# Kernel optimization log

Measured on AMD Instinct MI355X. Metric: run time of the kernel, lower is better.

Reference implementation:

```python
import jax, jax.numpy as jnp
import numpy as np
from jax import lax

C_IN, C_OUT, H, W = 64, 128, 512, 512


def setup_inputs() -> dict:
    key = jax.random.key(0)
    k1, k2, k3, k4 = jax.random.split(key, 4)
    x = jax.random.normal(k1, (C_IN, H, W), dtype=jnp.float32)
    # Conv2d params (eqx default: kernel 3x3, bias used). Small init scale for stability.
    conv_w = jax.random.normal(k2, (C_OUT, C_IN, 3, 3), dtype=jnp.float32) * 0.05
    conv_b = jax.random.normal(k3, (C_OUT,), dtype=jnp.float32) * 0.05
    fft_mask = jax.random.normal(k4, (C_OUT, H, W), dtype=jnp.float32)
    return {"x": x, "conv_w": conv_w, "conv_b": conv_b, "fft_mask": fft_mask}


def reference(x, conv_w, conv_b, fft_mask):
    # 3x3 same-padding conv on a single (C,H,W) sample -> (C_OUT,H,W)
    y = lax.conv_general_dilated(
        x[None],  # (1,C_IN,H,W)
        conv_w,
        window_strides=(1, 1),
        padding=((1, 1), (1, 1)),
        dimension_numbers=("NCHW", "OIHW", "NCHW"),
    )[0] + conv_b[:, None, None]
    # Per-channel spectral filter: FFT over (H,W), elementwise complex-mask
    # multiply, inverse FFT, take real part. Vectorized over channels.
    Y = jnp.fft.fftn(y, axes=(1, 2)) * fft_mask
    return jnp.fft.ifftn(Y, axes=(1, 2)).real
```

## Files before the change

### kernel.cpp

```cpp
#include <hip/hip_runtime.h>

#define CIN   64
#define COUT  128
#define HH    512
#define WW    512
#define HW    (HH*WW)

typedef __attribute__((ext_vector_type(8))) short  short8;
typedef __attribute__((ext_vector_type(4))) float  floatx4;


__device__ __forceinline__ unsigned short f2bf(float f) {
    unsigned u = __float_as_uint(f);
    u += 0x7fffu + ((u >> 16) & 1u);
    return (unsigned short)(u >> 16);
}

__device__ __forceinline__ void wave_sync() {
    __builtin_amdgcn_wave_barrier();
    asm volatile("s_waitcnt lgkmcnt(0)" ::: "memory");
    __builtin_amdgcn_sched_barrier(0);
}
template<bool BLK> __device__ __forceinline__ void xsync() {
    if (BLK) __syncthreads(); else wave_sync();
}


__global__ __launch_bounds__(256) void k_wprep(
        const float* __restrict__ cw,
        unsigned short* __restrict__ wt)
{
    int i = blockIdx.x * 256 + threadIdx.x;
    int tap = i >> 13;
    int co  = (i >> 6) & 127;
    int ci  = i & 63;
    wt[i] = f2bf(cw[(co * 64 + ci) * 9 + tap]);
}


__global__ __launch_bounds__(256) void k_xprep(
        const float* __restrict__ x,
        unsigned short* __restrict__ xt)
{
    __shared__ unsigned short tile[64][72];
    int t  = threadIdx.x;
    int h  = blockIdx.x >> 3;
    int w0 = (blockIdx.x & 7) << 6;
    int wl = t & 63;
#pragma unroll
    for (int it = 0; it < 16; ++it) {
        int ci = (t >> 6) + 4 * it;
        tile[wl][ci] = f2bf(x[ci * HW + h * 512 + w0 + wl]);
    }
    __syncthreads();
#pragma unroll
    for (int it = 0; it < 2; ++it) {
        int task = t + 256 * it;
        int w = task >> 3, seg = task & 7;
        *(short8*)&xt[((size_t)(h * 512 + w0 + w)) * 64 + seg * 8] =
            *(const short8*)&tile[w][seg * 8];
    }
}


__global__ __launch_bounds__(256) void k_maskT2(
        const float* __restrict__ mask,
        float* __restrict__ mt)
{
    __shared__ float t1[64][65];
    __shared__ float t2[64][65];
    int b  = blockIdx.x;
    int ch = b >> 6;
    int k0 = ((b >> 3) & 7) << 6;
    int c0 = (b & 7) << 6;
    int t  = threadIdx.x;
    int j  = t & 63, i0 = t >> 6;
    const float* mch = mask + (size_t)ch * HW;
#pragma unroll
    for (int it = 0; it < 16; ++it) {
        int i  = i0 + 4 * it;
        int mi = (512 - (k0 + i)) & 511;
        int mj = (512 - (c0 + j)) & 511;
        t1[i][j] = mch[(size_t)(k0 + i) * 512 + (c0 + j)];
        t2[i][j] = mch[(size_t)mi * 512 + mj];
    }
    __syncthreads();
    float* och = mt + (size_t)ch * HW;
#pragma unroll
    for (int it = 0; it < 16; ++it) {
        int jj = i0 + 4 * it;
        och[(size_t)(c0 + jj) * 512 + k0 + j] = t1[j][jj] + t2[j][jj];
    }
}


__global__ __launch_bounds__(512) void k_conv(
        const unsigned short* __restrict__ xt,
        const unsigned short* __restrict__ wt,
        const float* __restrict__ bias,
        float* __restrict__ y)
{
    __shared__ __align__(16) unsigned short As[3][130][68];

    int b  = blockIdx.x;
    int h  = b >> 2;
    int w0 = (b & 3) << 7;
    int t  = threadIdx.x;
    int lane = t & 63, wv = t >> 6;
    int wm = wv >> 2, wn = wv & 3;
    int l15 = lane & 15, quad = lane >> 4;

    for (int idx = t; idx < 3 * 130 * 8; idx += 512) {
        int dy  = idx / 1040;
        int rem = idx - dy * 1040;
        int p   = rem >> 3, seg = rem & 7;
        int hp  = h + dy - 1;
        int wq  = w0 - 1 + p;
        short8 v = {0, 0, 0, 0, 0, 0, 0, 0};
        if ((unsigned)hp < 512u && (unsigned)wq < 512u)
            v = *(const short8*)&xt[((size_t)(hp * 512 + wq)) * 64 + seg * 8];
        *(short8*)&As[dy][p][seg * 8] = v;
    }
    __syncthreads();

    floatx4 acc[4][2];
#pragma unroll
    for (int mt = 0; mt < 4; ++mt)
#pragma unroll
        for (int nt = 0; nt < 2; ++nt) {
            floatx4 z = {0.f, 0.f, 0.f, 0.f};
            acc[mt][nt] = z;
        }

#pragma unroll
    for (int tap = 0; tap < 9; ++tap) {
        int dy = tap / 3, dx = tap - dy * 3;
        short8 bfr[2][2];
#pragma unroll
        for (int nt = 0; nt < 2; ++nt)
#pragma unroll
            for (int kc = 0; kc < 2; ++kc) {
                int co = wn * 32 + nt * 16 + l15;
                bfr[nt][kc] = *(const short8*)
                    &wt[(tap * 128 + co) * 64 + kc * 32 + quad * 8];
            }
#pragma unroll
        for (int kc = 0; kc < 2; ++kc) {
            int c0 = kc * 32 + quad * 8;
            short8 afr[4];
#pragma unroll
            for (int mt = 0; mt < 4; ++mt) {
                int row = wm * 64 + mt * 16 + l15 + dx;
                afr[mt] = *(const short8*)&As[dy][row][c0];
            }
#pragma unroll
            for (int mt = 0; mt < 4; ++mt)
#pragma unroll
                for (int nt = 0; nt < 2; ++nt)
                    acc[mt][nt] = __builtin_amdgcn_mfma_f32_16x16x32_bf16(
                        afr[mt], bfr[nt][kc], acc[mt][nt], 0, 0, 0);
        }
    }

#pragma unroll
    for (int nt = 0; nt < 2; ++nt) {
        int co = wn * 32 + nt * 16 + l15;
        float bv = bias[co];
#pragma unroll
        for (int mt = 0; mt < 4; ++mt) {
            floatx4 o = acc[mt][nt];
            o[0] += bv; o[1] += bv; o[2] += bv; o[3] += bv;
            int m = wm * 64 + mt * 16 + quad * 4;
            *(floatx4*)&y[co * HW + h * 512 + w0 + m] = o;
        }
    }
}


#define FS 576

__device__ __forceinline__ int slotf(int c, int a) {
    return c * FS + ((a + (a >> 3)) ^ c);
}
__device__ __forceinline__ int dr6(int v) {
    return (v >> 3) + 8 * (v & 7);
}

__device__ __forceinline__ float2 cadd(float2 a, float2 b){ return make_float2(a.x+b.x, a.y+b.y); }
__device__ __forceinline__ float2 csub(float2 a, float2 b){ return make_float2(a.x-b.x, a.y-b.y); }

template<int DIR> __device__ __forceinline__ float2 twmul(float2 a, float2 t){
    return (DIR > 0) ? make_float2(a.x*t.x - a.y*t.y, a.x*t.y + a.y*t.x)
                     : make_float2(a.x*t.x + a.y*t.y, a.y*t.x - a.x*t.y);
}
template<int DIR> __device__ __forceinline__ float2 mulJ(float2 a){
    return (DIR > 0) ? make_float2(a.y, -a.x) : make_float2(-a.y, a.x);
}

#define RSQRT2 0.70710678118654752f

template<int DIR> __device__ __forceinline__ void dft8(float2* x){
    float2 a0 = cadd(x[0], x[4]), b0 = csub(x[0], x[4]);
    float2 a1 = cadd(x[1], x[5]), b1 = csub(x[1], x[5]);
    float2 a2 = cadd(x[2], x[6]), b2 = csub(x[2], x[6]);
    float2 a3 = cadd(x[3], x[7]), b3 = csub(x[3], x[7]);
    b1 = (DIR > 0) ? make_float2((b1.x + b1.y)*RSQRT2, (b1.y - b1.x)*RSQRT2)
                   : make_float2((b1.x - b1.y)*RSQRT2, (b1.y + b1.x)*RSQRT2);
    b2 = mulJ<DIR>(b2);
    b3 = (DIR > 0) ? make_float2((b3.y - b3.x)*RSQRT2, -(b3.x + b3.y)*RSQRT2)
                   : make_float2(-(b3.x + b3.y)*RSQRT2, (b3.x - b3.y)*RSQRT2);
    float2 c0 = cadd(a0, a2), d0 = csub(a0, a2);
    float2 c1 = cadd(a1, a3), d1 = mulJ<DIR>(csub(a1, a3));
    x[0] = cadd(c0, c1); x[4] = csub(c0, c1);
    x[2] = cadd(d0, d1); x[6] = csub(d0, d1);
    float2 e0 = cadd(b0, b2), f0 = csub(b0, b2);
    float2 e1 = cadd(b1, b3), f1 = mulJ<DIR>(csub(b1, b3));
    x[1] = cadd(e0, e1); x[5] = csub(e0, e1);
    x[3] = cadd(f0, f1); x[7] = csub(f0, f1);
}

template<bool BLK>
__device__ __forceinline__ void fft512_fwd(float2 X[2][8], float2* buf,
                                           const float2* tw, int w, int c) {
#pragma unroll
    for (int b = 0; b < 2; ++b) {
        dft8<1>(X[b]);
        int g = w + 32*b;
#pragma unroll
        for (int k = 1; k < 8; ++k) X[b][k] = twmul<1>(X[b][k], tw[g*k]);
    }
#pragma unroll
    for (int b = 0; b < 2; ++b) {
        int g = w + 32*b;
#pragma unroll
        for (int k = 0; k < 8; ++k) buf[slotf(c, k*64 + g)] = X[b][k];
    }
    xsync<BLK>();
#pragma unroll
    for (int b = 0; b < 2; ++b) {
        int u = w + 32*b; int bs = (u >> 3)*64 + (u & 7);
#pragma unroll
        for (int g2 = 0; g2 < 8; ++g2) X[b][g2] = buf[slotf(c, bs + 8*g2)];
    }
#pragma unroll
    for (int b = 0; b < 2; ++b) {
        dft8<1>(X[b]);
        int g1 = (w + 32*b) & 7;
#pragma unroll
        for (int k = 1; k < 8; ++k) X[b][k] = twmul<1>(X[b][k], tw[8*g1*k]);
    }
    xsync<BLK>();
#pragma unroll
    for (int b = 0; b < 2; ++b) {
        int u = w + 32*b; int bs = (u >> 3)*64 + (u & 7);
#pragma unroll
        for (int k = 0; k < 8; ++k) buf[slotf(c, bs + 8*k)] = X[b][k];
    }
    xsync<BLK>();
#pragma unroll
    for (int b = 0; b < 2; ++b) {
        int v = w + 32*b;
#pragma unroll
        for (int g1 = 0; g1 < 8; ++g1) X[b][g1] = buf[slotf(c, 8*v + g1)];
    }
#pragma unroll
    for (int b = 0; b < 2; ++b) dft8<1>(X[b]);
}

template<bool BLK>
__device__ __forceinline__ void fft512_inv(float2 X[2][8], float2* buf,
                                           const float2* tw, int w, int c) {
#pragma unroll
    for (int b = 0; b < 2; ++b) dft8<-1>(X[b]);
    xsync<BLK>();
#pragma unroll
    for (int b = 0; b < 2; ++b) {
        int v = w + 32*b;
#pragma unroll
        for (int g1 = 0; g1 < 8; ++g1) buf[slotf(c, 8*v + g1)] = X[b][g1];
    }
    xsync<BLK>();
#pragma unroll
    for (int b = 0; b < 2; ++b) {
        int u = w + 32*b; int bs = (u >> 3)*64 + (u & 7);
#pragma unroll
        for (int k = 0; k < 8; ++k) X[b][k] = buf[slotf(c, bs + 8*k)];
    }
#pragma unroll
    for (int b = 0; b < 2; ++b) {
        int g1 = (w + 32*b) & 7;
#pragma unroll
        for (int k = 1; k < 8; ++k) X[b][k] = twmul<-1>(X[b][k], tw[8*g1*k]);
        dft8<-1>(X[b]);
    }
    xsync<BLK>();
#pragma unroll
    for (int b = 0; b < 2; ++b) {
        int u = w + 32*b; int bs = (u >> 3)*64 + (u & 7);
#pragma unroll
        for (int g2 = 0; g2 < 8; ++g2) buf[slotf(c, bs + 8*g2)] = X[b][g2];
    }
    xsync<BLK>();
#pragma unroll
    for (int b = 0; b < 2; ++b) {
        int g = w + 32*b;
#pragma unroll
        for (int k = 0; k < 8; ++k) X[b][k] = buf[slotf(c, k*64 + g)];
    }
#pragma unroll
    for (int b = 0; b < 2; ++b) {
        int g = w + 32*b;
#pragma unroll
        for (int k = 1; k < 8; ++k) X[b][k] = twmul<-1>(X[b][k], tw[g*k]);
        dft8<-1>(X[b]);
    }
}

__device__ __forceinline__ void build_tw(float2* tw, int t) {
    const float a0 = -6.283185307179586f / 512.0f;
    float s, c;
    __sincosf(a0 * (float)t, &s, &c);         tw[t]       = make_float2(c, s);
    __sincosf(a0 * (float)(t + 256), &s, &c); tw[t + 256] = make_float2(c, s);
}


__global__ __launch_bounds__(256, 4) void k_rows_fwd_pair(
        const float* __restrict__ y,
        float2* __restrict__ Z)
{
    __shared__ float2 buf[8 * FS];
    __shared__ float2 tw[512];
    int t = threadIdx.x;
    build_tw(tw, t);
    int c = t >> 5, w = t & 31;
    int p = blockIdx.x >> 6, r0 = (blockIdx.x & 63) << 3;
    const float* yA = y + (size_t)(2*p) * HW + (size_t)(r0 + c) * 512;
    const float* yB = yA + HW;

    float2 X[2][8];
#pragma unroll
    for (int b = 0; b < 2; ++b)
#pragma unroll
        for (int r = 0; r < 8; ++r) {
            int off = w + 32*b + 64*r;
            X[b][r] = make_float2(yA[off], yB[off]);
        }
    __syncthreads();
    fft512_fwd<false>(X, buf, tw, w, c);

    wave_sync();
#pragma unroll
    for (int b = 0; b < 2; ++b) {
        int kb = dr6(w + 32*b);
#pragma unroll
        for (int m = 0; m < 8; ++m) buf[slotf(c, kb + 64*m)] = X[b][m];
    }
    __syncthreads();
    size_t zb = (size_t)p * HW + r0;
    for (int it = 0; it < 16; ++it) {
        int n = t + 256*it;
        int col = n >> 3, rr = n & 7;
        Z[zb + (size_t)col*512 + rr] = buf[slotf(rr, col)];
    }
}

__device__ __forceinline__ int col_of(int g, int j) {
    if (g == 0) return (j < 4) ? j : (j == 4 ? 256 : 504 + j);
    return (j < 4) ? 4*g + j : 512 - 4*g - 7 + j;
}
__device__ __forceinline__ int jmir(int g, int j) {
    return (g == 0) ? ((8 - j) & 7) : (7 - j);
}

__global__ __launch_bounds__(256, 4) void k_cols_pair(
        float2* __restrict__ Z,
        const float* __restrict__ mt)
{
    __shared__ float2 buf[8 * FS];
    __shared__ float2 tw[512];
    int t = threadIdx.x;
    build_tw(tw, t);
    int c = t >> 5, w = t & 31;
    int p = blockIdx.x >> 6, g = blockIdx.x & 63;
    int colc = col_of(g, c);
    int cm   = jmir(g, c);
    size_t zcol = (size_t)p * HW + (size_t)colc * 512;
    const float* mAp = mt + (size_t)(2*p) * HW + (size_t)colc * 512;
    const float* mBp = mAp + HW;

    float2 X[2][8];
#pragma unroll
    for (int b = 0; b < 2; ++b)
#pragma unroll
        for (int r = 0; r < 8; ++r)
            X[b][r] = Z[zcol + w + 32*b + 64*r];
    float Sa[2][8], Sb[2][8];
#pragma unroll
    for (int b = 0; b < 2; ++b) {
        int kb = dr6(w + 32*b);
#pragma unroll
        for (int m = 0; m < 8; ++m) {
            int k1 = kb + 64*m;
            Sa[b][m] = mAp[k1];
            Sb[b][m] = mBp[k1];
        }
    }
    __syncthreads();
    fft512_fwd<false>(X, buf, tw, w, c);

    wave_sync();
#pragma unroll
    for (int b = 0; b < 2; ++b) {
        int kb = dr6(w + 32*b);
#pragma unroll
        for (int m = 0; m < 8; ++m) buf[slotf(c, kb + 64*m)] = X[b][m];
    }
    __syncthreads();

    const float s4 = 0.25f / 262144.0f;
#pragma unroll
    for (int b = 0; b < 2; ++b) {
        int kb = dr6(w + 32*b);
#pragma unroll
        for (int m = 0; m < 8; ++m) {
            int k1  = kb + 64*m;
            int mk1 = (512 - k1) & 511;
            float2 P = X[b][m];
            float2 Q = buf[slotf(cm, mk1)];
            float alpha = (Sa[b][m] + Sb[b][m]) * s4;
            float beta  = (Sa[b][m] - Sb[b][m]) * s4;
            X[b][m] = make_float2(alpha * P.x + beta * Q.x,
                                  alpha * P.y - beta * Q.y);
        }
    }
    __syncthreads();
    fft512_inv<false>(X, buf, tw, w, c);
#pragma unroll
    for (int b = 0; b < 2; ++b)
#pragma unroll
        for (int r = 0; r < 8; ++r)
            Z[zcol + w + 32*b + 64*r] = X[b][r];
}

__global__ __launch_bounds__(256, 4) void k_rows_inv_pair(
        const float2* __restrict__ Z,
        float* __restrict__ out)
{
    __shared__ float2 buf[8 * FS];
    __shared__ float2 tw[512];
    int t = threadIdx.x;
    build_tw(tw, t);
    int c = t >> 5, w = t & 31;
    int p = blockIdx.x >> 6, r0 = (blockIdx.x & 63) << 3;
    size_t zb = (size_t)p * HW + r0;

    for (int it = 0; it < 16; ++it) {
        int n = t + 256*it;
        int col = n >> 3, rr = n & 7;
        buf[slotf(rr, col)] = Z[zb + (size_t)col*512 + rr];
    }
    __syncthreads();

    float2 X[2][8];
#pragma unroll
    for (int b = 0; b < 2; ++b) {
        int kb = dr6(w + 32*b);
#pragma unroll
        for (int m = 0; m < 8; ++m) X[b][m] = buf[slotf(c, kb + 64*m)];
    }
    fft512_inv<false>(X, buf, tw, w, c);

    float* oA = out + (size_t)(2*p) * HW + (size_t)(r0 + c) * 512;
    float* oB = oA + HW;
#pragma unroll
    for (int b = 0; b < 2; ++b)
#pragma unroll
        for (int r = 0; r < 8; ++r) {
            int off = w + 32*b + 64*r;
            oA[off] = X[b][r].x;
            oB[off] = X[b][r].y;
        }
}


extern "C" void kernel_launch(void* const* d_in, const int* in_sizes, int n_in,
                              void* d_out, int out_size, void* d_ws, size_t ws_size,
                              hipStream_t stream) {
    const float* x    = (const float*)d_in[0];
    const float* cw   = (const float*)d_in[1];
    const float* cb   = (const float*)d_in[2];
    const float* mask = (const float*)d_in[3];

    float*  outRe = (float*)d_out;
    float2* ZT    = (float2*)d_ws;

    unsigned short* xt = (unsigned short*)d_ws;
    unsigned short* wt = (unsigned short*)d_ws + (size_t)HW * 64;

    k_wprep<<<288, 256, 0, stream>>>(cw, wt);
    k_xprep<<<4096, 256, 0, stream>>>(x, xt);
    k_conv<<<2048, 512, 0, stream>>>(xt, wt, cb, outRe);
    k_rows_fwd_pair<<<4096, 256, 0, stream>>>(outRe, ZT);
    k_maskT2<<<8192, 256, 0, stream>>>(mask, outRe);
    k_cols_pair<<<4096, 256, 0, stream>>>(ZT, outRe);
    k_rows_inv_pair<<<4096, 256, 0, stream>>>(ZT, outRe);
}
```

Baseline: 659.5 us.

## Widen row FFT blocks to 16 rows and stage column FFT I/O through LDS

```diff
diff --git a/kernel.cpp b/kernel.cpp
--- a/kernel.cpp
+++ b/kernel.cpp
@@ -316,84 +316,87 @@
     }
 }
 
+template<int NT>
 __device__ __forceinline__ void build_tw(float2* tw, int t) {
     const float a0 = -6.283185307179586f / 512.0f;
-    float s, c;
-    __sincosf(a0 * (float)t, &s, &c);         tw[t]       = make_float2(c, s);
-    __sincosf(a0 * (float)(t + 256), &s, &c); tw[t + 256] = make_float2(c, s);
-}
-
-
-__global__ __launch_bounds__(256, 4) void k_rows_fwd_pair(
+#pragma unroll
+    for (int i = 0; i < 512/NT; ++i) {
+        float s, c;
+        __sincosf(a0 * (float)(t + NT*i), &s, &c);
+        tw[t + NT*i] = make_float2(c, s);
+    }
+}
+
+
+__global__ __launch_bounds__(512) void k_rows_fwd_pair(
         const float* __restrict__ y,
         float2* __restrict__ Z)
+{
+    __shared__ float2 buf[16 * FS];
+    __shared__ float2 tw[512];
+    int t = threadIdx.x;
+    build_tw<512>(tw, t);
+    int c = t >> 5, w = t & 31;
+    int p = blockIdx.x >> 5, r0 = (blockIdx.x & 31) << 4;
+    const float* yA = y + (size_t)(2*p) * HW + (size_t)(r0 + c) * 512;
+    const float* yB = yA + HW;
+
+    float2 X[2][8];
+#pragma unroll
+    for (int b = 0; b < 2; ++b)
+#pragma unroll
+        for (int r = 0; r < 8; ++r) {
+            int off = w + 32*b + 64*r;
+            X[b][r] = make_float2(yA[off], yB[off]);
+        }
+    __syncthreads();
+    fft512_fwd<false>(X, buf, tw, w, c);
+
+    wave_sync();
+#pragma unroll
+    for (int b = 0; b < 2; ++b) {
+        int kb = dr6(w + 32*b);
+#pragma unroll
+        for (int m = 0; m < 8; ++m) buf[slotf(c, kb + 64*m)] = X[b][m];
+    }
+    __syncthreads();
+    size_t zb = (size_t)p * HW + r0;
+    for (int it = 0; it < 16; ++it) {
+        int n = t + 512*it;
+        int col = n >> 4, rr = n & 15;
+        Z[zb + (size_t)col*512 + rr] = buf[slotf(rr, col)];
+    }
+}
+
+__device__ __forceinline__ int col_of(int g, int j) {
+    if (g == 0) return (j < 4) ? j : (j == 4 ? 256 : 504 + j);
+    return (j < 4) ? 4*g + j : 512 - 4*g - 7 + j;
+}
+__device__ __forceinline__ int jmir(int g, int j) {
+    return (g == 0) ? ((8 - j) & 7) : (7 - j);
+}
+
+__global__ __launch_bounds__(256, 4) void k_cols_pair(
+        float2* __restrict__ Z,
+        const float* __restrict__ mt)
 {
     __shared__ float2 buf[8 * FS];
     __shared__ float2 tw[512];
     int t = threadIdx.x;
-    build_tw(tw, t);
-    int c = t >> 5, w = t & 31;
-    int p = blockIdx.x >> 6, r0 = (blockIdx.x & 63) << 3;
-    const float* yA = y + (size_t)(2*p) * HW + (size_t)(r0 + c) * 512;
-    const float* yB = yA + HW;
-
-    float2 X[2][8];
-#pragma unroll
-    for (int b = 0; b < 2; ++b)
-#pragma unroll
-        for (int r = 0; r < 8; ++r) {
-            int off = w + 32*b + 64*r;
-            X[b][r] = make_float2(yA[off], yB[off]);
-        }
-    __syncthreads();
-    fft512_fwd<false>(X, buf, tw, w, c);
-
-    wave_sync();
-#pragma unroll
-    for (int b = 0; b < 2; ++b) {
-        int kb = dr6(w + 32*b);
-#pragma unroll
-        for (int m = 0; m < 8; ++m) buf[slotf(c, kb + 64*m)] = X[b][m];
-    }
-    __syncthreads();
-    size_t zb = (size_t)p * HW + r0;
-    for (int it = 0; it < 16; ++it) {
-        int n = t + 256*it;
-        int col = n >> 3, rr = n & 7;
-        Z[zb + (size_t)col*512 + rr] = buf[slotf(rr, col)];
-    }
-}
-
-__device__ __forceinline__ int col_of(int g, int j) {
-    if (g == 0) return (j < 4) ? j : (j == 4 ? 256 : 504 + j);
-    return (j < 4) ? 4*g + j : 512 - 4*g - 7 + j;
-}
-__device__ __forceinline__ int jmir(int g, int j) {
-    return (g == 0) ? ((8 - j) & 7) : (7 - j);
-}
-
-__global__ __launch_bounds__(256, 4) void k_cols_pair(
-        float2* __restrict__ Z,
-        const float* __restrict__ mt)
-{
-    __shared__ float2 buf[8 * FS];
-    __shared__ float2 tw[512];
-    int t = threadIdx.x;
-    build_tw(tw, t);
+    build_tw<256>(tw, t);
     int c = t >> 5, w = t & 31;
     int p = blockIdx.x >> 6, g = blockIdx.x & 63;
     int colc = col_of(g, c);
     int cm   = jmir(g, c);
-    size_t zcol = (size_t)p * HW + (size_t)colc * 512;
+    size_t zch = (size_t)p * HW;
     const float* mAp = mt + (size_t)(2*p) * HW + (size_t)colc * 512;
     const float* mBp = mAp + HW;
 
-    float2 X[2][8];
-#pragma unroll
-    for (int b = 0; b < 2; ++b)
-#pragma unroll
-        for (int r = 0; r < 8; ++r)
-            X[b][r] = Z[zcol + w + 32*b + 64*r];
+    for (int it = 0; it < 16; ++it) {
+        int n = t + 256*it;
+        int cj = n >> 9, row = n & 511;
+        buf[slotf(cj, row)] = Z[zch + (size_t)col_of(g, cj)*512 + row];
+    }
     float Sa[2][8], Sb[2][8];
 #pragma unroll
     for (int b = 0; b < 2; ++b) {
@@ -406,6 +409,14 @@
         }
     }
     __syncthreads();
+
+    float2 X[2][8];
+#pragma unroll
+    for (int b = 0; b < 2; ++b)
+#pragma unroll
+        for (int r = 0; r < 8; ++r)
+            X[b][r] = buf[slotf(c, w + 32*b + 64*r)];
+    wave_sync();
     fft512_fwd<false>(X, buf, tw, w, c);
 
     wave_sync();
@@ -435,28 +446,35 @@
     }
     __syncthreads();
     fft512_inv<false>(X, buf, tw, w, c);
+    wave_sync();
 #pragma unroll
     for (int b = 0; b < 2; ++b)
 #pragma unroll
         for (int r = 0; r < 8; ++r)
-            Z[zcol + w + 32*b + 64*r] = X[b][r];
-}
-
-__global__ __launch_bounds__(256, 4) void k_rows_inv_pair(
+            buf[slotf(c, w + 32*b + 64*r)] = X[b][r];
+    __syncthreads();
+    for (int it = 0; it < 16; ++it) {
+        int n = t + 256*it;
+        int cj = n >> 9, row = n & 511;
+        Z[zch + (size_t)col_of(g, cj)*512 + row] = buf[slotf(cj, row)];
+    }
+}
+
+__global__ __launch_bounds__(512) void k_rows_inv_pair(
         const float2* __restrict__ Z,
         float* __restrict__ out)
 {
-    __shared__ float2 buf[8 * FS];
+    __shared__ float2 buf[16 * FS];
     __shared__ float2 tw[512];
     int t = threadIdx.x;
-    build_tw(tw, t);
+    build_tw<512>(tw, t);
     int c = t >> 5, w = t & 31;
-    int p = blockIdx.x >> 6, r0 = (blockIdx.x & 63) << 3;
+    int p = blockIdx.x >> 5, r0 = (blockIdx.x & 31) << 4;
     size_t zb = (size_t)p * HW + r0;
 
     for (int it = 0; it < 16; ++it) {
-        int n = t + 256*it;
-        int col = n >> 3, rr = n & 7;
+        int n = t + 512*it;
+        int col = n >> 4, rr = n & 15;
         buf[slotf(rr, col)] = Z[zb + (size_t)col*512 + rr];
     }
     __syncthreads();
@@ -500,8 +518,8 @@
     k_wprep<<<288, 256, 0, stream>>>(cw, wt);
     k_xprep<<<4096, 256, 0, stream>>>(x, xt);
     k_conv<<<2048, 512, 0, stream>>>(xt, wt, cb, outRe);
-    k_rows_fwd_pair<<<4096, 256, 0, stream>>>(outRe, ZT);
+    k_rows_fwd_pair<<<2048, 512, 0, stream>>>(outRe, ZT);
     k_maskT2<<<8192, 256, 0, stream>>>(mask, outRe);
     k_cols_pair<<<4096, 256, 0, stream>>>(ZT, outRe);
-    k_rows_inv_pair<<<4096, 256, 0, stream>>>(ZT, outRe);
-}
+    k_rows_inv_pair<<<2048, 512, 0, stream>>>(ZT, outRe);
+}
```

Result: slower. 683.7 us (+3.7%).
